# Kernel tuning notes

Hardware: AMD Instinct MI355X
Metric: run time of the kernel (lower is better)

The kernel has to match this reference:

```python
import jax, jax.numpy as jnp
import numpy as np

HIDDEN = 768
NUM_HEADS = 8
NUM_CELLS = 16384
MAX_HDRS = 8
NUM_HEADERS = 512
LN_EPS = 1e-5


def setup_inputs() -> dict:
    key = jax.random.key(0)
    ks = jax.random.split(key, 16)
    s = 0.02
    D = HIDDEN
    return {
        "cell_value_embeddings": jax.random.normal(ks[0], (NUM_CELLS, D), jnp.float32),
        "header_embeddings": jax.random.normal(ks[1], (NUM_HEADERS, D), jnp.float32),
        "cell_to_header_map": jax.random.randint(ks[2], (NUM_CELLS, MAX_HDRS), 0, NUM_HEADERS),
        "cell_positions": jax.random.randint(ks[3], (NUM_CELLS, 2), 0, 100),
        # nn.MultiheadAttention params
        "in_proj_w": jax.random.normal(ks[4], (3 * D, D), jnp.float32) * s,
        "in_proj_b": jnp.zeros((3 * D,), jnp.float32),
        "out_w": jax.random.normal(ks[5], (D, D), jnp.float32) * s,
        "out_b": jnp.zeros((D,), jnp.float32),
        # positional embedding tables
        "row_emb": jax.random.normal(ks[6], (100, D), jnp.float32) * s,
        "col_emb": jax.random.normal(ks[7], (100, D), jnp.float32) * s,
        # fusion: Linear(2D->D) + LayerNorm
        "fus_w": jax.random.normal(ks[8], (D, 2 * D), jnp.float32) * s,
        "fus_b": jnp.zeros((D,), jnp.float32),
        "ln_g": jnp.ones((D,), jnp.float32),
        "ln_b": jnp.zeros((D,), jnp.float32),
    }


def _forward(cell_value_embeddings, header_embeddings, in_proj_w, in_proj_b,
             out_w, out_b, row_emb, col_emb, fus_w, fus_b, ln_g, ln_b,
             cell_to_header_map, cell_positions):
    N, D = cell_value_embeddings.shape
    H = cell_to_header_map.shape[1]
    nh, dh = NUM_HEADS, D // NUM_HEADS
    scale = 1.0 / (dh ** 0.5)

    pos = jnp.clip(cell_positions, 0, 99)
    cwp = cell_value_embeddings + row_emb[pos[:, 0]] + col_emb[pos[:, 1]]  # [N,D]

    ids = cell_to_header_map
    mask = ids >= 0                                   # [N,H] valid header slots
    hg = header_embeddings[jnp.where(mask, ids, 0)]   # [N,H,D] gathered K/V inputs

    Wq, Wk, Wv = jnp.split(in_proj_w, 3, axis=0)
    bq, bk, bv = jnp.split(in_proj_b, 3)
    q = (cwp @ Wq.T + bq).reshape(N, nh, dh)          # [N,a,d]
    k = (hg @ Wk.T + bk).reshape(N, H, nh, dh)        # [N,k,a,d]
    v = (hg @ Wv.T + bv).reshape(N, H, nh, dh)

    scores = jnp.einsum('nad,nkad->nak', q, k) * scale          # [N,a,k]
    scores = jnp.where(mask[:, None, :], scores, -1e9)
    attn = jax.nn.softmax(scores, axis=-1)
    attn = jnp.where(mask[:, None, :], attn, 0.0)
    ctx = jnp.einsum('nak,nkad->nad', attn, v).reshape(N, D)
    att_out = ctx @ out_w.T + out_b                    # [N,D]

    comb = jnp.concatenate([cwp, att_out], axis=-1)    # [N,2D]
    h = comb @ fus_w.T + fus_b
    mu = jnp.mean(h, axis=-1, keepdims=True)
    var = jnp.mean((h - mu) ** 2, axis=-1, keepdims=True)
    h = (h - mu) * jax.lax.rsqrt(var + LN_EPS) * ln_g + ln_b
    fused = jax.nn.relu(h)

    has = jnp.any(mask, axis=-1)                       # cells with >=1 valid header
    enriched = jnp.where(has[:, None], fused, cwp)
    weights = jnp.where(mask, attn.mean(axis=1), 0.0)  # head-averaged attn [N,H]
    return enriched, weights


def reference(cell_value_embeddings, header_embeddings, cell_to_header_map,
              cell_positions, in_proj_w, in_proj_b, out_w, out_b, row_emb,
              col_emb, fus_w, fus_b, ln_g, ln_b):
    return _forward(cell_value_embeddings, header_embeddings, in_proj_w,
                    in_proj_b, out_w, out_b, row_emb, col_emb, fus_w, fus_b,
                    ln_g, ln_b, cell_to_header_map, cell_positions)
```

## Files before the change

### kernel.cpp

```cpp
#include <hip/hip_runtime.h>
#include <hip/hip_bf16.h>

#define NCELLS 16384
#define DIM    768
#define NHEADS 8
#define DHEAD  96
#define MAXH   8
#define ND     (NCELLS * DIM)


using bf16 = __hip_bfloat16;
typedef short  short8  __attribute__((ext_vector_type(8)));
typedef short  short4v __attribute__((ext_vector_type(4)));
typedef float  floatx4 __attribute__((ext_vector_type(4)));

__device__ inline short f2b(float f) {
    bf16 h = __float2bfloat16(f);
    unsigned short u; __builtin_memcpy(&u, &h, 2); return (short)u;
}
__device__ inline float b2f(short u) {
    unsigned x = ((unsigned)(unsigned short)u) << 16;
    float f; __builtin_memcpy(&f, &x, 4); return f;
}

__device__ inline short8 ld8(const float* p) {
    floatx4 a = *reinterpret_cast<const floatx4*>(p);
    floatx4 b = *reinterpret_cast<const floatx4*>(p + 4);
    short8 o;
#pragma unroll
    for (int i = 0; i < 4; ++i) { o[i] = f2b(a[i]); o[i + 4] = f2b(b[i]); }
    return o;
}

__device__ __forceinline__ void cp16(const void* g, void* l) {
    __builtin_amdgcn_global_load_lds(
        (const __attribute__((address_space(1))) void*)g,
        (__attribute__((address_space(3))) void*)l, 16, 0, 0);
}

template <int DUAL, int COUT>
__global__ __launch_bounds__(256) void gemm_bf(
    const bf16* __restrict__ A, const bf16* __restrict__ A2,
    const bf16* __restrict__ W, int ldw,
    const float* __restrict__ bias,
    float* __restrict__ Cf, bf16* __restrict__ Cb, int K)
{
    __shared__ short As[128 * 64];
    __shared__ short Bs[128 * 64];
    const int tid = threadIdx.x, wave = tid >> 6, lane = tid & 63;
    const int id = blockIdx.x;
    const int m0 = (id & 127) * 128;
    const int n0 = (id >> 7) * 128;
    const int wr = (wave & 1) * 64, wc = (wave >> 1) * 64;
    const int fr = lane & 15, kg = lane >> 4;

    const int srow = lane >> 3;
    const int scol = (lane & 7) ^ srow;

    floatx4 acc[16];
#pragma unroll
    for (int i = 0; i < 16; ++i) acc[i] = (floatx4){0.f, 0.f, 0.f, 0.f};

    for (int k0 = 0; k0 < K; k0 += 64) {
        const bf16* Ak; int ka;
        if (!DUAL || k0 < DIM) { Ak = A;  ka = k0; }
        else                   { Ak = A2; ka = k0 - DIM; }

        __syncthreads();
#pragma unroll
        for (int i = 0; i < 4; ++i) {
            const int c = i * 4 + wave;
            const int row = c * 8 + srow;
            cp16(Ak + (size_t)(m0 + row) * DIM + ka + scol * 8,
                 &As[c * 512 + lane * 8]);
            cp16(W  + (size_t)(n0 + row) * ldw + k0 + scol * 8,
                 &Bs[c * 512 + lane * 8]);
        }
        __syncthreads();

#pragma unroll
        for (int kk = 0; kk < 2; ++kk) {
            short8 af[4], bfv[4];
#pragma unroll
            for (int i = 0; i < 4; ++i) {
                const int sa = ((kk * 4 + kg) ^ (fr & 7)) * 8;
                af[i]  = *reinterpret_cast<const short8*>(&As[(wr + i * 16 + fr) * 64 + sa]);
                bfv[i] = *reinterpret_cast<const short8*>(&Bs[(wc + i * 16 + fr) * 64 + sa]);
            }
#pragma unroll
            for (int i = 0; i < 4; ++i)
#pragma unroll
                for (int j = 0; j < 4; ++j)
                    acc[i * 4 + j] = __builtin_amdgcn_mfma_f32_16x16x32_bf16(
                        af[i], bfv[j], acc[i * 4 + j], 0, 0, 0);
        }
    }

    const int col_l = lane & 15, row_q = kg * 4;
#pragma unroll
    for (int j = 0; j < 4; ++j) {
        const int col = n0 + wc + j * 16 + col_l;
        const float bv = bias[col];
#pragma unroll
        for (int i = 0; i < 4; ++i) {
#pragma unroll
            for (int r = 0; r < 4; ++r) {
                const int row = m0 + wr + i * 16 + row_q + r;
                const float v = acc[i * 4 + j][r] + bv;
                if (COUT == 0) Cf[(size_t)row * DIM + col] = v;
                else           Cb[(size_t)row * DIM + col] = __float2bfloat16(v);
            }
        }
    }
}

__global__ __launch_bounds__(256) void prep_kernel(
    const float* __restrict__ ce, const int* __restrict__ pos,
    const float* __restrict__ re, const float* __restrict__ co,
    bf16* __restrict__ cwp_b,
    const float* __restrict__ in_proj_w, bf16* __restrict__ Wq_b,
    const float* __restrict__ out_w,     bf16* __restrict__ Wo_b,
    const float* __restrict__ fus_w,     bf16* __restrict__ Wf_b,
    const float* __restrict__ hdr, const float* __restrict__ in_proj_b,
    bf16* __restrict__ HKV)
{
    __shared__ short As[64 * 40];
    __shared__ short Bs[64 * 40];
    const int b = blockIdx.x, tid = threadIdx.x;

    if (b < 6144) {
        const int gid  = b * 256 + tid;
        const int cell = gid / 96;
        const int off  = (gid % 96) * 8;
        int pr = pos[cell * 2 + 0]; pr = min(max(pr, 0), 99);
        int pc = pos[cell * 2 + 1]; pc = min(max(pc, 0), 99);
        const float* a = ce + (size_t)cell * DIM + off;
        const float* bb = re + (size_t)pr * DIM + off;
        const float* c = co + (size_t)pc * DIM + off;
        floatx4 a0 = *reinterpret_cast<const floatx4*>(a);
        floatx4 a1 = *reinterpret_cast<const floatx4*>(a + 4);
        floatx4 b0 = *reinterpret_cast<const floatx4*>(bb);
        floatx4 b1 = *reinterpret_cast<const floatx4*>(bb + 4);
        floatx4 c0 = *reinterpret_cast<const floatx4*>(c);
        floatx4 c1 = *reinterpret_cast<const floatx4*>(c + 4);
        short8 o;
#pragma unroll
        for (int i = 0; i < 4; ++i) {
            o[i]     = f2b(a0[i] + b0[i] + c0[i]);
            o[i + 4] = f2b(a1[i] + b1[i] + c1[i]);
        }
        *reinterpret_cast<short8*>((short*)cwp_b + (size_t)cell * DIM + off) = o;
    } else if (b < 8448) {
        const float* src; bf16* dst; int i;
        if (b < 6720)      { src = in_proj_w; dst = Wq_b; i = (b - 6144) * 256 + tid; }
        else if (b < 7296) { src = out_w;     dst = Wo_b; i = (b - 6720) * 256 + tid; }
        else               { src = fus_w;     dst = Wf_b; i = (b - 7296) * 256 + tid; }
        floatx4 v = *reinterpret_cast<const floatx4*>(src + (size_t)i * 4);
        short4v o;
#pragma unroll
        for (int j = 0; j < 4; ++j) o[j] = f2b(v[j]);
        *reinterpret_cast<short4v*>((short*)dst + (size_t)i * 4) = o;
    } else {
        const int b2 = b - 8448;
        const int m0 = (b2 & 7) * 64, n0 = (b2 >> 3) * 64;
        const float* W = in_proj_w + (size_t)DIM * DIM;
        const float* bias = in_proj_b + DIM;
        const int wave = tid >> 6, lane = tid & 63;
        const int lr = tid >> 2, lc = (tid & 3) * 8;
        const int fr = lane & 15, fk = (lane >> 4) * 8;

        floatx4 acc[4];
#pragma unroll
        for (int i = 0; i < 4; ++i) acc[i] = (floatx4){0.f, 0.f, 0.f, 0.f};

        for (int k0 = 0; k0 < DIM; k0 += 32) {
            short8 av = ld8(hdr + (size_t)(m0 + lr) * DIM + k0 + lc);
            short8 wv = ld8(W   + (size_t)(n0 + lr) * DIM + k0 + lc);
            __syncthreads();
            *reinterpret_cast<short8*>(&As[lr * 40 + lc]) = av;
            *reinterpret_cast<short8*>(&Bs[lr * 40 + lc]) = wv;
            __syncthreads();
            short8 af = *reinterpret_cast<const short8*>(&As[(wave * 16 + fr) * 40 + fk]);
#pragma unroll
            for (int t = 0; t < 4; ++t) {
                short8 bfv = *reinterpret_cast<const short8*>(&Bs[(t * 16 + fr) * 40 + fk]);
                acc[t] = __builtin_amdgcn_mfma_f32_16x16x32_bf16(af, bfv, acc[t], 0, 0, 0);
            }
        }
        const int col_l = lane & 15, row_q = (lane >> 4) * 4;
#pragma unroll
        for (int t = 0; t < 4; ++t) {
            const int col = n0 + t * 16 + col_l;
            const float bv = bias[col];
#pragma unroll
            for (int r = 0; r < 4; ++r) {
                const int row = m0 + wave * 16 + row_q + r;
                HKV[(size_t)row * 1536 + col] = __float2bfloat16(acc[t][r] + bv);
            }
        }
    }
}

__global__ __launch_bounds__(256) void attn_v_kernel(
    const bf16* __restrict__ q, bf16* __restrict__ ctx,
    const bf16* __restrict__ HKV, const int* __restrict__ map,
    float* __restrict__ wout)
{
    const int h = threadIdx.x >> 7;
    const int t = threadIdx.x & 127;
    const int cell = blockIdx.x * 2 + h;
    __shared__ float qs[2][DIM];
    __shared__ float sc[2][64];
    __shared__ float at[2][64];
    __shared__ int   ids[2][MAXH];
    __shared__ float msk[2][MAXH];

    if (t < MAXH) {
        int id = map[cell * MAXH + t];
        msk[h][t] = (id >= 0) ? 1.f : 0.f;
        ids[h][t] = (id >= 0) ? id : 0;
    }
    if (t < 96) {
        short8 qv = *reinterpret_cast<const short8*>((const short*)q + (size_t)cell * DIM + t * 8);
#pragma unroll
        for (int e = 0; e < 8; ++e) qs[h][t * 8 + e] = b2f(qv[e]);
    }
    __syncthreads();

    if (t < 64) {
        const int a = t >> 3, j = t & 7;
        const short* kp = (const short*)HKV + (size_t)ids[h][j] * 1536 + a * DHEAD;
        float s = 0.f;
#pragma unroll
        for (int c = 0; c < 12; ++c) {
            short8 kv = *reinterpret_cast<const short8*>(kp + c * 8);
#pragma unroll
            for (int e = 0; e < 8; ++e)
                s += qs[h][a * DHEAD + c * 8 + e] * b2f(kv[e]);
        }
        s *= 0.10206207261596577f;
        sc[h][t] = (msk[h][j] != 0.f) ? s : -1e9f;
    }
    __syncthreads();

    if (t < NHEADS) {
        float m = -3e38f;
        for (int j = 0; j < MAXH; ++j) m = fmaxf(m, sc[h][t * 8 + j]);
        float e[MAXH]; float sum = 0.f;
        for (int j = 0; j < MAXH; ++j) { e[j] = expf(sc[h][t * 8 + j] - m); sum += e[j]; }
        const float inv = 1.f / sum;
        for (int j = 0; j < MAXH; ++j)
            at[h][t * 8 + j] = (msk[h][j] != 0.f) ? e[j] * inv : 0.f;
    }
    __syncthreads();

    if (t < MAXH) {
        float s = 0.f;
        for (int a = 0; a < NHEADS; ++a) s += at[h][a * 8 + t];
        wout[(size_t)cell * MAXH + t] = s * 0.125f;
    }

    if (t < 96) {
        const int a = t / 12, d0 = t * 8;
        float acc[8];
#pragma unroll
        for (int e = 0; e < 8; ++e) acc[e] = 0.f;
#pragma unroll
        for (int j = 0; j < MAXH; ++j) {
            short8 vv = *reinterpret_cast<const short8*>(
                (const short*)HKV + (size_t)ids[h][j] * 1536 + DIM + d0);
            const float w = at[h][a * 8 + j];
#pragma unroll
            for (int e = 0; e < 8; ++e) acc[e] += w * b2f(vv[e]);
        }
        short8 o;
#pragma unroll
        for (int e = 0; e < 8; ++e) o[e] = f2b(acc[e]);
        *reinterpret_cast<short8*>((short*)ctx + (size_t)cell * DIM + d0) = o;
    }
}

__global__ __launch_bounds__(384) void ln_v_kernel(
    float* io, const int* __restrict__ map,
    const float* __restrict__ ce, const int* __restrict__ pos,
    const float* __restrict__ re, const float* __restrict__ co,
    const float* __restrict__ g, const float* __restrict__ b)
{
    const int h = threadIdx.x / 192;
    const int t = threadIdx.x % 192;
    const int cell = blockIdx.x * 2 + h;
    const int wave = t >> 6, lane = t & 63;
    __shared__ float ws_[2][3], wq_[2][3];
    __shared__ int hasf[2];
    if (threadIdx.x < 2) hasf[threadIdx.x] = 0;

    float* hp = io + (size_t)cell * DIM;
    floatx4 v = *reinterpret_cast<const floatx4*>(hp + t * 4);
    float s  = v[0] + v[1] + v[2] + v[3];
    float q2 = v[0]*v[0] + v[1]*v[1] + v[2]*v[2] + v[3]*v[3];
#pragma unroll
    for (int off = 32; off > 0; off >>= 1) {
        s  += __shfl_down(s, off);
        q2 += __shfl_down(q2, off);
    }
    __syncthreads();
    if (t < MAXH && map[cell * MAXH + t] >= 0) hasf[h] = 1;
    if (lane == 0) { ws_[h][wave] = s; wq_[h][wave] = q2; }
    __syncthreads();

    const float mu  = (ws_[h][0] + ws_[h][1] + ws_[h][2]) * (1.f / 768.f);
    const float var = (wq_[h][0] + wq_[h][1] + wq_[h][2]) * (1.f / 768.f) - mu * mu;
    const float inv = rsqrtf(var + 1e-5f);

    if (hasf[h]) {
        floatx4 gv = *reinterpret_cast<const floatx4*>(g + t * 4);
        floatx4 bv = *reinterpret_cast<const floatx4*>(b + t * 4);
        floatx4 o;
#pragma unroll
        for (int e = 0; e < 4; ++e)
            o[e] = fmaxf((v[e] - mu) * inv * gv[e] + bv[e], 0.f);
        *reinterpret_cast<floatx4*>(hp + t * 4) = o;
    } else {
        int pr = pos[cell * 2 + 0]; pr = min(max(pr, 0), 99);
        int pc = pos[cell * 2 + 1]; pc = min(max(pc, 0), 99);
        floatx4 a0 = *reinterpret_cast<const floatx4*>(ce + (size_t)cell * DIM + t * 4);
        floatx4 b0 = *reinterpret_cast<const floatx4*>(re + (size_t)pr * DIM + t * 4);
        floatx4 c0 = *reinterpret_cast<const floatx4*>(co + (size_t)pc * DIM + t * 4);
        floatx4 o;
#pragma unroll
        for (int e = 0; e < 4; ++e) o[e] = a0[e] + b0[e] + c0[e];
        *reinterpret_cast<floatx4*>(hp + t * 4) = o;
    }
}

extern "C" void kernel_launch(void* const* d_in, const int* in_sizes, int n_in,
                              void* d_out, int out_size, void* d_ws, size_t ws_size,
                              hipStream_t stream) {
    (void)in_sizes; (void)n_in; (void)out_size; (void)ws_size;

    const float* cell_emb  = (const float*)d_in[0];
    const float* hdr_emb   = (const float*)d_in[1];
    const int*   map       = (const int*)d_in[2];
    const int*   pos       = (const int*)d_in[3];
    const float* in_proj_w = (const float*)d_in[4];
    const float* in_proj_b = (const float*)d_in[5];
    const float* out_w     = (const float*)d_in[6];
    const float* out_b     = (const float*)d_in[7];
    const float* row_emb   = (const float*)d_in[8];
    const float* col_emb   = (const float*)d_in[9];
    const float* fus_w     = (const float*)d_in[10];
    const float* fus_b     = (const float*)d_in[11];
    const float* ln_g      = (const float*)d_in[12];
    const float* ln_b      = (const float*)d_in[13];
    float* out = (float*)d_out;

    char* ws = (char*)d_ws;
    bf16* HKV    = (bf16*)ws;
    bf16* att_b  = (bf16*)(ws + 1572864);
    bf16* cwp_b  = (bf16*)(ws + 26738688);
    bf16* Wq_b   = (bf16*)(ws + 51904512);
    bf16* Wo_b   = (bf16*)(ws + 53084160);
    bf16* Wf_b   = (bf16*)(ws + 54263808);
    bf16* q_b    = (bf16*)d_out;
    bf16* ctx_b  = (bf16*)((char*)d_out + 25165824);

    prep_kernel<<<8640, 256, 0, stream>>>(
        cell_emb, pos, row_emb, col_emb, cwp_b,
        in_proj_w, Wq_b, out_w, Wo_b, fus_w, Wf_b,
        hdr_emb, in_proj_b, HKV);

    gemm_bf<0, 1><<<768, 256, 0, stream>>>(
        cwp_b, nullptr, Wq_b, DIM, in_proj_b, nullptr, q_b, DIM);

    attn_v_kernel<<<NCELLS / 2, 256, 0, stream>>>(q_b, ctx_b, HKV, map, out + ND);

    gemm_bf<0, 1><<<768, 256, 0, stream>>>(
        ctx_b, nullptr, Wo_b, DIM, out_b, nullptr, att_b, DIM);

    gemm_bf<1, 0><<<768, 256, 0, stream>>>(
        cwp_b, att_b, Wf_b, 1536, fus_b, out, nullptr, 1536);

    ln_v_kernel<<<NCELLS / 2, 384, 0, stream>>>(out, map, cell_emb, pos,
                                                row_emb, col_emb, ln_g, ln_b);
}
```

Before: 306.8 us.

## Fold output projection into fusion weights to drop one GEMM

Precomputes Wf2·Wo, the right half of the fusion weight multiplied by the attention output projection, as a small 768x768 GEMM inside the prep kernel. The folded bias Wf2·out_b + fus_b is computed there too, so the fusion GEMM consumes ctx directly. This removes a full 16384x768x768 GEMM launch and the att_b intermediate round trip. The cost is a small extra weight GEMM per call that uses strided, uncoalesced out_w loads, plus different bf16 rounding because the product of the two weights is rounded once.

```diff
diff --git a/kernel.cpp b/kernel.cpp
--- a/kernel.cpp
+++ b/kernel.cpp
@@ -119,8 +119,9 @@
     const float* __restrict__ re, const float* __restrict__ co,
     bf16* __restrict__ cwp_b,
     const float* __restrict__ in_proj_w, bf16* __restrict__ Wq_b,
-    const float* __restrict__ out_w,     bf16* __restrict__ Wo_b,
-    const float* __restrict__ fus_w,     bf16* __restrict__ Wf_b,
+    const float* __restrict__ fus_w,     bf16* __restrict__ W_cat,
+    const float* __restrict__ out_w,     const float* __restrict__ out_b,
+    const float* __restrict__ fus_b,     float* __restrict__ biasp,
     const float* __restrict__ hdr, const float* __restrict__ in_proj_b,
     bf16* __restrict__ HKV)
 {
@@ -150,18 +151,23 @@
             o[i + 4] = f2b(a1[i] + b1[i] + c1[i]);
         }
         *reinterpret_cast<short8*>((short*)cwp_b + (size_t)cell * DIM + off) = o;
-    } else if (b < 8448) {
-        const float* src; bf16* dst; int i;
-        if (b < 6720)      { src = in_proj_w; dst = Wq_b; i = (b - 6144) * 256 + tid; }
-        else if (b < 7296) { src = out_w;     dst = Wo_b; i = (b - 6720) * 256 + tid; }
-        else               { src = fus_w;     dst = Wf_b; i = (b - 7296) * 256 + tid; }
-        floatx4 v = *reinterpret_cast<const floatx4*>(src + (size_t)i * 4);
+    } else if (b < 6720) {
+        const int i = (b - 6144) * 256 + tid;
+        floatx4 v = *reinterpret_cast<const floatx4*>(in_proj_w + (size_t)i * 4);
         short4v o;
 #pragma unroll
         for (int j = 0; j < 4; ++j) o[j] = f2b(v[j]);
-        *reinterpret_cast<short4v*>((short*)dst + (size_t)i * 4) = o;
-    } else {
-        const int b2 = b - 8448;
+        *reinterpret_cast<short4v*>((short*)Wq_b + (size_t)i * 4) = o;
+    } else if (b < 7296) {
+        const int i = (b - 6720) * 256 + tid;
+        const int n = i / 192, j = (i % 192) * 4;
+        floatx4 v = *reinterpret_cast<const floatx4*>(fus_w + (size_t)n * 1536 + j);
+        short4v o;
+#pragma unroll
+        for (int e = 0; e < 4; ++e) o[e] = f2b(v[e]);
+        *reinterpret_cast<short4v*>((short*)W_cat + (size_t)n * 1536 + j) = o;
+    } else if (b < 7488) {
+        const int b2 = b - 7296;
         const int m0 = (b2 & 7) * 64, n0 = (b2 >> 3) * 64;
         const float* W = in_proj_w + (size_t)DIM * DIM;
         const float* bias = in_proj_b + DIM;
@@ -172,7 +178,6 @@
         floatx4 acc[4];
 #pragma unroll
         for (int i = 0; i < 4; ++i) acc[i] = (floatx4){0.f, 0.f, 0.f, 0.f};
-
         for (int k0 = 0; k0 < DIM; k0 += 32) {
             short8 av = ld8(hdr + (size_t)(m0 + lr) * DIM + k0 + lc);
             short8 wv = ld8(W   + (size_t)(n0 + lr) * DIM + k0 + lc);
@@ -197,6 +202,59 @@
                 const int row = m0 + wave * 16 + row_q + r;
                 HKV[(size_t)row * 1536 + col] = __float2bfloat16(acc[t][r] + bv);
             }
+        }
+    } else if (b < 7632) {
+        const int b2 = b - 7488;
+        const int n0 = (b2 % 12) * 64, j0 = (b2 / 12) * 64;
+        const int wave = tid >> 6, lane = tid & 63;
+        const int lr = tid >> 2, lc = (tid & 3) * 8;
+        const int fr = lane & 15, fk = (lane >> 4) * 8;
+
+        floatx4 acc[4];
+#pragma unroll
+        for (int i = 0; i < 4; ++i) acc[i] = (floatx4){0.f, 0.f, 0.f, 0.f};
+        for (int k0 = 0; k0 < DIM; k0 += 32) {
+            short8 av = ld8(fus_w + (size_t)(n0 + lr) * 1536 + DIM + k0 + lc);
+            float tmp[8];
+#pragma unroll
+            for (int i = 0; i < 8; ++i)
+                tmp[i] = out_w[(size_t)(k0 + lc + i) * DIM + j0 + lr];
+            short8 wv;
+#pragma unroll
+            for (int i = 0; i < 8; ++i) wv[i] = f2b(tmp[i]);
+            __syncthreads();
+            *reinterpret_cast<short8*>(&As[lr * 40 + lc]) = av;
+            *reinterpret_cast<short8*>(&Bs[lr * 40 + lc]) = wv;
+            __syncthreads();
+            short8 af = *reinterpret_cast<const short8*>(&As[(wave * 16 + fr) * 40 + fk]);
+#pragma unroll
+            for (int t = 0; t < 4; ++t) {
+                short8 bfv = *reinterpret_cast<const short8*>(&Bs[(t * 16 + fr) * 40 + fk]);
+                acc[t] = __builtin_amdgcn_mfma_f32_16x16x32_bf16(af, bfv, acc[t], 0, 0, 0);
+            }
+        }
+        const int col_l = lane & 15, row_q = (lane >> 4) * 4;
+#pragma unroll
+        for (int t = 0; t < 4; ++t) {
+            const int j = j0 + t * 16 + col_l;
+#pragma unroll
+            for (int r = 0; r < 4; ++r) {
+                const int n = n0 + wave * 16 + row_q + r;
+                W_cat[(size_t)n * 1536 + DIM + j] = __float2bfloat16(acc[t][r]);
+            }
+        }
+    } else {
+#pragma unroll
+        for (int rr = 0; rr < 3; ++rr) {
+            const int n = tid + rr * 256;
+            float s = fus_b[n];
+            const float* wrow = fus_w + (size_t)n * 1536 + DIM;
+            for (int k = 0; k < DIM; k += 4) {
+                floatx4 wv = *reinterpret_cast<const floatx4*>(wrow + k);
+                floatx4 bv = *reinterpret_cast<const floatx4*>(out_b + k);
+                s += wv[0]*bv[0] + wv[1]*bv[1] + wv[2]*bv[2] + wv[3]*bv[3];
+            }
+            biasp[n] = s;
         }
     }
 }
@@ -355,18 +413,17 @@
     float* out = (float*)d_out;
 
     char* ws = (char*)d_ws;
-    bf16* HKV    = (bf16*)ws;
-    bf16* att_b  = (bf16*)(ws + 1572864);
-    bf16* cwp_b  = (bf16*)(ws + 26738688);
-    bf16* Wq_b   = (bf16*)(ws + 51904512);
-    bf16* Wo_b   = (bf16*)(ws + 53084160);
-    bf16* Wf_b   = (bf16*)(ws + 54263808);
-    bf16* q_b    = (bf16*)d_out;
-    bf16* ctx_b  = (bf16*)((char*)d_out + 25165824);
-
-    prep_kernel<<<8640, 256, 0, stream>>>(
+    bf16*  HKV   = (bf16*)ws;
+    bf16*  ctx_b = (bf16*)(ws + 1572864);
+    bf16*  cwp_b = (bf16*)(ws + 26738688);
+    bf16*  Wq_b  = (bf16*)(ws + 51904512);
+    bf16*  W_cat = (bf16*)(ws + 53084160);
+    float* biasp = (float*)(ws + 55443456);
+    bf16*  q_b   = (bf16*)d_out;
+
+    prep_kernel<<<7633, 256, 0, stream>>>(
         cell_emb, pos, row_emb, col_emb, cwp_b,
-        in_proj_w, Wq_b, out_w, Wo_b, fus_w, Wf_b,
+        in_proj_w, Wq_b, fus_w, W_cat, out_w, out_b, fus_b, biasp,
         hdr_emb, in_proj_b, HKV);
 
     gemm_bf<0, 1><<<768, 256, 0, stream>>>(
@@ -374,11 +431,8 @@
 
     attn_v_kernel<<<NCELLS / 2, 256, 0, stream>>>(q_b, ctx_b, HKV, map, out + ND);
 
-    gemm_bf<0, 1><<<768, 256, 0, stream>>>(
-        ctx_b, nullptr, Wo_b, DIM, out_b, nullptr, att_b, DIM);
-
     gemm_bf<1, 0><<<768, 256, 0, stream>>>(
-        cwp_b, att_b, Wf_b, 1536, fus_b, out, nullptr, 1536);
+        cwp_b, ctx_b, W_cat, 1536, biasp, out, nullptr, 1536);
 
     ln_v_kernel<<<NCELLS / 2, 384, 0, stream>>>(out, map, cell_emb, pos,
                                                 row_emb, col_emb, ln_g, ln_b);
```

New measurement: 333.0 us. 8.5% more time.
